# Kernel optimization log

Measured on AMD Instinct MI355X. Metric: run time of the kernel, lower is better.

The kernel has to match this reference:

```python
import jax, jax.numpy as jnp
import numpy as np

N, E, B = 50000, 800000, 128
IN, HID, OUT, H = 256, 256, 256, 4
NEG_SLOPE = 0.2
EPS_BN = 1e-5
EPS_LN = 1e-5


def setup_inputs() -> dict:
    key = jax.random.key(0)
    ks = jax.random.split(key, 10)
    C1, C2 = HID // H, OUT // H
    s = lambda k, sh: jax.random.normal(k, sh, jnp.float32) * 0.05
    return dict(
        x=jax.random.normal(ks[0], (N, IN), jnp.float32),
        edge_index=jax.random.randint(ks[1], (2, E), 0, N),
        batch=jnp.sort(jax.random.randint(ks[2], (N,), 0, B)),
        W1=s(ks[3], (IN, HID)), a_src1=s(ks[4], (H, C1)), a_dst1=s(ks[5], (H, C1)),
        b1=jnp.zeros((HID,), jnp.float32),
        bn1_g=jnp.ones((HID,), jnp.float32), bn1_b=jnp.zeros((HID,), jnp.float32),
        bn1_m=jnp.zeros((HID,), jnp.float32), bn1_v=jnp.ones((HID,), jnp.float32),
        ln1_g=jnp.ones((HID,), jnp.float32), ln1_b=jnp.zeros((HID,), jnp.float32),
        W2=s(ks[6], (HID + IN, OUT)), a_src2=s(ks[7], (H, C2)), a_dst2=s(ks[8], (H, C2)),
        b2=jnp.zeros((OUT,), jnp.float32),
        bn2_g=jnp.ones((OUT,), jnp.float32), bn2_b=jnp.zeros((OUT,), jnp.float32),
        bn2_m=jnp.zeros((OUT,), jnp.float32), bn2_v=jnp.ones((OUT,), jnp.float32),
        ln2_g=jnp.ones((OUT,), jnp.float32), ln2_b=jnp.zeros((OUT,), jnp.float32),
    )


def gat_conv(x, edge_index, W, a_s, a_d, b):
    # PyG GATConv (concat heads, add_self_loops=True, eval -> no attention dropout)
    n = x.shape[0]
    Hh, C = a_s.shape
    h = (x @ W).reshape(n, Hh, C)                      # [N,H,C]
    loop = jnp.arange(n)
    src = jnp.concatenate([edge_index[0], loop])       # [E+N]
    dst = jnp.concatenate([edge_index[1], loop])
    al_s = jnp.einsum('nhc,hc->nh', h, a_s)            # [N,H]
    al_d = jnp.einsum('nhc,hc->nh', h, a_d)
    e = jax.nn.leaky_relu(al_s[src] + al_d[dst], NEG_SLOPE)   # [E+N,H]
    emax = jax.ops.segment_max(e, dst, num_segments=n)        # segment softmax over incoming edges
    p = jnp.exp(e - emax[dst])
    denom = jax.ops.segment_sum(p, dst, num_segments=n)
    alpha = p / (denom[dst] + 1e-16)
    out = jax.ops.segment_sum(alpha[:, :, None] * h[src], dst, num_segments=n)
    return out.reshape(n, Hh * C) + b


def bn_eval(x, g, b, m, v):
    return (x - m) * (g * jax.lax.rsqrt(v + EPS_BN)) + b


def layer_norm(x, g, b):
    mu = jnp.mean(x, axis=-1, keepdims=True)
    var = jnp.mean(jnp.square(x - mu), axis=-1, keepdims=True)
    return (x - mu) * jax.lax.rsqrt(var + EPS_LN) * g + b


def reference(x, edge_index, batch,
              W1, a_src1, a_dst1, b1, bn1_g, bn1_b, bn1_m, bn1_v, ln1_g, ln1_b,
              W2, a_src2, a_dst2, b2, bn2_g, bn2_b, bn2_m, bn2_v, ln2_g, ln2_b):
    x1 = x
    h = gat_conv(x, edge_index, W1, a_src1, a_dst1, b1)
    h = jax.nn.relu(layer_norm(bn_eval(h, bn1_g, bn1_b, bn1_m, bn1_v), ln1_g, ln1_b))
    x2 = h
    # root_extend: broadcast the first node of each (sorted) batch segment
    root_idx = jnp.searchsorted(batch, jnp.arange(B))  # first occurrence per graph
    h = jnp.concatenate([h, x1[root_idx[batch]]], axis=1)
    h = gat_conv(h, edge_index, W2, a_src2, a_dst2, b2)
    h = jax.nn.relu(layer_norm(bn_eval(h, bn2_g, bn2_b, bn2_m, bn2_v), ln2_g, ln2_b))
    h = jnp.concatenate([h, x2[root_idx[batch]]], axis=1)   # [N, OUT+HID]
    sums = jax.ops.segment_sum(h, batch, num_segments=B)
    cnt = jax.ops.segment_sum(jnp.ones((h.shape[0],), h.dtype), batch, num_segments=B)
    return sums / jnp.maximum(cnt, 1.0)[:, None]            # scatter_mean -> [B, OUT+HID]
```

## Files before the change

kernel.cpp:

```cpp
#include <hip/hip_runtime.h>
#include <stdint.h>

typedef unsigned short u16;
typedef unsigned int u32;
typedef __bf16 bf16x8 __attribute__((ext_vector_type(8)));
typedef float f32x4 __attribute__((ext_vector_type(4)));

#define NGRAPH 128

__device__ __forceinline__ float b2f(u16 u) {
    union { u32 i; float f; } c; c.i = ((u32)u) << 16; return c.f;
}
__device__ __forceinline__ u16 f2b(float f) {
    union { float f; u32 i; } c; c.f = f;
    u32 r = c.i + 0x7fffu + ((c.i >> 16) & 1u);
    return (u16)(r >> 16);
}

__global__ void k_sentinel(u16* __restrict__ out, int n, u16 pat) {
    int i = blockIdx.x * 256 + threadIdx.x;
    if (i < n) out[i] = pat;
}

__global__ void k_detect(const u16* __restrict__ x, int* __restrict__ flag) {
    __shared__ int cnt;
    if (threadIdx.x == 0) cnt = 0;
    __syncthreads();
    int weird = 0;
    for (int i = threadIdx.x; i < 4096; i += 256) {
        u16 u = x[2 * i];
        int e = (u >> 7) & 0xff;
        if (e != 0 && (e < 100 || e > 140)) weird++;
    }
    atomicAdd(&cnt, weird);
    __syncthreads();
    if (threadIdx.x == 0) *flag = (cnt > 1024) ? 1 : 0;
}

__global__ __launch_bounds__(256) void k_cvt(const void* __restrict__ src, u16* __restrict__ dst,
                                             int n, const int* __restrict__ flag) {
    int f = *flag;
    int i = blockIdx.x * 256 + threadIdx.x;
    if (i < n) dst[i] = f ? f2b(((const float*)src)[i]) : ((const u16*)src)[i];
}

__global__ __launch_bounds__(256) void k_cvt_small(
    const void* p0, const void* p1, const void* p2, const void* p3, const void* p4,
    const void* p5, const void* p6, const void* p7, const void* p8, const void* p9,
    const void* p10, const void* p11, const void* p12, const void* p13, const void* p14,
    const void* p15, const void* p16, const void* p17,
    u16* __restrict__ dst, const int* __restrict__ flag) {
    const void* ps[18] = {p0,p1,p2,p3,p4,p5,p6,p7,p8,p9,p10,p11,p12,p13,p14,p15,p16,p17};
    int f = *flag;
    int vec = blockIdx.x;
    int j = threadIdx.x;
    const void* s = ps[vec];
    dst[vec * 256 + j] = f ? f2b(((const float*)s)[j]) : ((const u16*)s)[j];
}

__global__ void k_zero(int* __restrict__ deg, float* __restrict__ pool, int nd, int np) {
    int i = blockIdx.x * blockDim.x + threadIdx.x;
    if (i < nd) deg[i] = 0;
    if (i < np) pool[i] = 0.0f;
}

__global__ void k_transpose(const u16* __restrict__ w, u16* __restrict__ wt) {
    int idx = blockIdx.x * 256 + threadIdx.x;
    int n = idx >> 8, k = idx & 255;
    wt[n * 256 + k] = w[k * 256 + n];
}

__global__ void k_root(const int* __restrict__ batch, int* __restrict__ root, int N, int B) {
    int b = threadIdx.x;
    if (b > B) return;
    int lo = 0, hi = N;
    while (lo < hi) { int mid = (lo + hi) >> 1; if (batch[mid] < b) lo = mid + 1; else hi = mid; }
    root[b] = lo;
}

__global__ __launch_bounds__(256) void k_hist(const int* __restrict__ ei, int* __restrict__ deg, int E) {
    int e = blockIdx.x * 256 + threadIdx.x;
    if (e < E) atomicAdd(&deg[ei[E + e]], 1);
}

__global__ __launch_bounds__(256) void k_scan1(const int* __restrict__ in, int* __restrict__ out,
                                               int* __restrict__ bsums, int total) {
    __shared__ int lds[256];
    int tid = threadIdx.x;
    int base = blockIdx.x * 2048 + tid * 8;
    int v[8]; int ts = 0;
#pragma unroll
    for (int r = 0; r < 8; r++) { int i = base + r; int x = (i < total) ? in[i] : 0; v[r] = x; ts += x; }
    lds[tid] = ts;
    __syncthreads();
    for (int off = 1; off < 256; off <<= 1) {
        int t = (tid >= off) ? lds[tid - off] : 0;
        __syncthreads();
        lds[tid] += t;
        __syncthreads();
    }
    int run = lds[tid] - ts;
#pragma unroll
    for (int r = 0; r < 8; r++) { int i = base + r; if (i < total) out[i] = run; run += v[r]; }
    if (tid == 255) bsums[blockIdx.x] = lds[255];
}

__global__ void k_scan2(int* __restrict__ bsums, int nb) {
    if (threadIdx.x == 0 && blockIdx.x == 0) {
        int run = 0;
        for (int i = 0; i < nb; i++) { int t = bsums[i]; bsums[i] = run; run += t; }
    }
}

__global__ __launch_bounds__(256) void k_scan3(const int* __restrict__ pscan, const int* __restrict__ bsums,
                                               int* __restrict__ ptr, int* __restrict__ cursor,
                                               int total, int N) {
    int i = blockIdx.x * 256 + threadIdx.x;
    if (i >= total) return;
    int val = pscan[i] + bsums[i >> 11];
    ptr[i] = val;
    if (i < N) cursor[i] = val;
}

__global__ __launch_bounds__(256) void k_fill(const int* __restrict__ ei, int* __restrict__ cursor,
                                              int* __restrict__ csr, int E) {
    int e = blockIdx.x * 256 + threadIdx.x;
    if (e < E) {
        int src = ei[e];
        int pos = atomicAdd(&cursor[ei[E + e]], 1);
        csr[pos] = src;
    }
}

__global__ __launch_bounds__(256) void k_gemm(const u16* __restrict__ A, const u16* __restrict__ Bt,
                                              u16* __restrict__ C, int M,
                                              const float* __restrict__ r2, const int* __restrict__ batch) {
    __shared__ __align__(16) u16 As[128 * 64];
    __shared__ __align__(16) u16 Bs[128 * 64];
    const int tid = threadIdx.x;
    const int lane = tid & 63;
    const int wave = tid >> 6;
    const int bm = blockIdx.x >> 1;
    const int bn = blockIdx.x & 1;
    const int m0 = bm * 128, n0 = bn * 128;
    const int wm = wave >> 1, wn = wave & 1;
    const int lm = lane & 15, lq = lane >> 4;
    f32x4 acc[4][4] = {};

    for (int k0 = 0; k0 < 256; k0 += 64) {
        uint4 ra[4], rb[4];
#pragma unroll
        for (int it = 0; it < 4; ++it) {
            int t = tid + 256 * it;
            int m = t >> 3;
            int kc = (t & 7) ^ (m & 7);
            int gm = m0 + m; if (gm > M - 1) gm = M - 1;
            ra[it] = *(const uint4*)(A + (size_t)gm * 256 + k0 + kc * 8);
            rb[it] = *(const uint4*)(Bt + (size_t)(n0 + m) * 256 + k0 + kc * 8);
        }
        __syncthreads();
#pragma unroll
        for (int it = 0; it < 4; ++it) {
            int t = tid + 256 * it;
            *(uint4*)(As + t * 8) = ra[it];
            *(uint4*)(Bs + t * 8) = rb[it];
        }
        __syncthreads();
#pragma unroll
        for (int ks = 0; ks < 2; ++ks) {
            int kq = ks * 4 + lq;
            bf16x8 af[4], bfr[4];
#pragma unroll
            for (int i = 0; i < 4; i++) {
                int m = wm * 64 + i * 16 + lm;
                af[i] = *(const bf16x8*)(As + (m * 8 + (kq ^ (m & 7))) * 8);
                int n = wn * 64 + i * 16 + lm;
                bfr[i] = *(const bf16x8*)(Bs + (n * 8 + (kq ^ (n & 7))) * 8);
            }
#pragma unroll
            for (int i = 0; i < 4; i++)
#pragma unroll
                for (int j = 0; j < 4; j++)
                    acc[i][j] = __builtin_amdgcn_mfma_f32_16x16x32_bf16(af[i], bfr[j], acc[i][j], 0, 0, 0);
        }
    }
#pragma unroll
    for (int i = 0; i < 4; i++) {
#pragma unroll
        for (int r = 0; r < 4; r++) {
            int row = m0 + wm * 64 + i * 16 + lq * 4 + r;
            if (row >= M) continue;
            const float* r2row = r2 ? (r2 + (size_t)batch[row] * 256) : nullptr;
#pragma unroll
            for (int j = 0; j < 4; j++) {
                int col = n0 + wn * 64 + j * 16 + lm;
                float v = acc[i][j][r];
                if (r2row) v += r2row[col];
                C[(size_t)row * 256 + col] = f2b(v);
            }
        }
    }
}

__global__ __launch_bounds__(256) void k_al(const u16* __restrict__ h, const u16* __restrict__ a_s,
                                            const u16* __restrict__ a_d,
                                            float* __restrict__ al_s, float* __restrict__ al_d, int N) {
    int node = blockIdx.x * 4 + (threadIdx.x >> 6);
    if (node >= N) return;
    int lane = threadIdx.x & 63;
    int c0 = lane * 4;
    int head = lane >> 4;
    int ci = c0 & 63;
    ushort4 hv = *(const ushort4*)(h + (size_t)node * 256 + c0);
    float h0 = b2f(hv.x), h1 = b2f(hv.y), h2 = b2f(hv.z), h3 = b2f(hv.w);
    ushort4 sv = *(const ushort4*)(a_s + head * 64 + ci);
    ushort4 dv = *(const ushort4*)(a_d + head * 64 + ci);
    float ps = h0 * b2f(sv.x) + h1 * b2f(sv.y) + h2 * b2f(sv.z) + h3 * b2f(sv.w);
    float pd = h0 * b2f(dv.x) + h1 * b2f(dv.y) + h2 * b2f(dv.z) + h3 * b2f(dv.w);
#pragma unroll
    for (int off = 1; off < 16; off <<= 1) { ps += __shfl_xor(ps, off); pd += __shfl_xor(pd, off); }
    if ((lane & 15) == 0) { al_s[node * 4 + head] = ps; al_d[node * 4 + head] = pd; }
}

__global__ __launch_bounds__(256) void k_attw(
    const float* __restrict__ als, const float* __restrict__ ald_,
    const int* __restrict__ ptr, const int* __restrict__ csr,
    float* __restrict__ aw, float* __restrict__ selfp, float* __restrict__ invs, int N) {
    int node = blockIdx.x * 4 + (threadIdx.x >> 6);
    if (node >= N) return;
    int lane = threadIdx.x & 63;
    int hd = lane & 3;
    int el = lane >> 2;
    int beg = ptr[node], end = ptr[node + 1];
    float ad = ald_[node * 4 + hd];
    float es = als[node * 4 + hd] + ad; es = (es > 0.f) ? es : 0.2f * es;
    float m = es;
    for (int i0 = beg; i0 < end; i0 += 16) {
        int i = i0 + el;
        if (i < end) {
            int src = csr[i];
            float e2 = als[src * 4 + hd] + ad; e2 = (e2 > 0.f) ? e2 : 0.2f * e2;
            m = fmaxf(m, e2);
        }
    }
#pragma unroll
    for (int off = 4; off < 64; off <<= 1) m = fmaxf(m, __shfl_xor(m, off));
    float s = 0.f;
    for (int i0 = beg; i0 < end; i0 += 16) {
        int i = i0 + el;
        if (i < end) {
            int src = csr[i];
            float e2 = als[src * 4 + hd] + ad; e2 = (e2 > 0.f) ? e2 : 0.2f * e2;
            float p = __expf(e2 - m);
            aw[(size_t)i * 4 + hd] = p;
            s += p;
        }
    }
#pragma unroll
    for (int off = 4; off < 64; off <<= 1) s += __shfl_xor(s, off);
    float pself = __expf(es - m);
    s += pself;
    if (el == 0) {
        float inv = 1.0f / (s + 1e-16f);
        selfp[node * 4 + hd] = pself * inv;
        invs[node * 4 + hd] = inv;
    }
}

__global__ __launch_bounds__(256) void k_agg2(
    const u16* __restrict__ h, const float* __restrict__ aw,
    const float* __restrict__ selfp, const float* __restrict__ invs,
    const int* __restrict__ ptr, const int* __restrict__ csr,
    const u16* __restrict__ bias, const u16* __restrict__ bng, const u16* __restrict__ bnb,
    const u16* __restrict__ bnm, const u16* __restrict__ bnv,
    const u16* __restrict__ lng, const u16* __restrict__ lnb,
    u16* __restrict__ xout, float* __restrict__ pool, const int* __restrict__ batch, int N) {
    int node = blockIdx.x * 4 + (threadIdx.x >> 6);
    if (node >= N) return;
    int lane = threadIdx.x & 63;
    int c0 = lane * 4;
    int head = lane >> 4;
    int beg = ptr[node], end = ptr[node + 1];
    float a0 = 0.f, a1 = 0.f, a2 = 0.f, a3 = 0.f;
    int i = beg;
    for (; i + 4 <= end; i += 4) {
        int s0 = csr[i], s1 = csr[i + 1], s2 = csr[i + 2], s3 = csr[i + 3];
        float p0 = aw[(size_t)i * 4 + head];
        float p1 = aw[(size_t)(i + 1) * 4 + head];
        float p2 = aw[(size_t)(i + 2) * 4 + head];
        float p3 = aw[(size_t)(i + 3) * 4 + head];
        ushort4 r0 = *(const ushort4*)(h + (size_t)s0 * 256 + c0);
        ushort4 r1 = *(const ushort4*)(h + (size_t)s1 * 256 + c0);
        ushort4 r2v = *(const ushort4*)(h + (size_t)s2 * 256 + c0);
        ushort4 r3 = *(const ushort4*)(h + (size_t)s3 * 256 + c0);
        a0 += p0 * b2f(r0.x) + p1 * b2f(r1.x) + p2 * b2f(r2v.x) + p3 * b2f(r3.x);
        a1 += p0 * b2f(r0.y) + p1 * b2f(r1.y) + p2 * b2f(r2v.y) + p3 * b2f(r3.y);
        a2 += p0 * b2f(r0.z) + p1 * b2f(r1.z) + p2 * b2f(r2v.z) + p3 * b2f(r3.z);
        a3 += p0 * b2f(r0.w) + p1 * b2f(r1.w) + p2 * b2f(r2v.w) + p3 * b2f(r3.w);
    }
    for (; i < end; ++i) {
        int s0 = csr[i];
        float p0 = aw[(size_t)i * 4 + head];
        ushort4 r0 = *(const ushort4*)(h + (size_t)s0 * 256 + c0);
        a0 += p0 * b2f(r0.x); a1 += p0 * b2f(r0.y); a2 += p0 * b2f(r0.z); a3 += p0 * b2f(r0.w);
    }
    float inv = invs[node * 4 + head];
    float sp = selfp[node * 4 + head];
    ushort4 hs = *(const ushort4*)(h + (size_t)node * 256 + c0);
    float v0 = a0 * inv + sp * b2f(hs.x) + b2f(bias[c0 + 0]);
    float v1 = a1 * inv + sp * b2f(hs.y) + b2f(bias[c0 + 1]);
    float v2 = a2 * inv + sp * b2f(hs.z) + b2f(bias[c0 + 2]);
    float v3 = a3 * inv + sp * b2f(hs.w) + b2f(bias[c0 + 3]);
    v0 = (v0 - b2f(bnm[c0 + 0])) * (b2f(bng[c0 + 0]) * rsqrtf(b2f(bnv[c0 + 0]) + 1e-5f)) + b2f(bnb[c0 + 0]);
    v1 = (v1 - b2f(bnm[c0 + 1])) * (b2f(bng[c0 + 1]) * rsqrtf(b2f(bnv[c0 + 1]) + 1e-5f)) + b2f(bnb[c0 + 1]);
    v2 = (v2 - b2f(bnm[c0 + 2])) * (b2f(bng[c0 + 2]) * rsqrtf(b2f(bnv[c0 + 2]) + 1e-5f)) + b2f(bnb[c0 + 2]);
    v3 = (v3 - b2f(bnm[c0 + 3])) * (b2f(bng[c0 + 3]) * rsqrtf(b2f(bnv[c0 + 3]) + 1e-5f)) + b2f(bnb[c0 + 3]);
    float sum = v0 + v1 + v2 + v3;
#pragma unroll
    for (int off = 1; off < 64; off <<= 1) sum += __shfl_xor(sum, off);
    float mu = sum * 0.00390625f;
    float d0 = v0 - mu, d1 = v1 - mu, d2 = v2 - mu, d3 = v3 - mu;
    float q = d0 * d0 + d1 * d1 + d2 * d2 + d3 * d3;
#pragma unroll
    for (int off = 1; off < 64; off <<= 1) q += __shfl_xor(q, off);
    float rstd = rsqrtf(q * 0.00390625f + 1e-5f);
    float y0 = fmaxf(d0 * rstd * b2f(lng[c0 + 0]) + b2f(lnb[c0 + 0]), 0.f);
    float y1 = fmaxf(d1 * rstd * b2f(lng[c0 + 1]) + b2f(lnb[c0 + 1]), 0.f);
    float y2 = fmaxf(d2 * rstd * b2f(lng[c0 + 2]) + b2f(lnb[c0 + 2]), 0.f);
    float y3 = fmaxf(d3 * rstd * b2f(lng[c0 + 3]) + b2f(lnb[c0 + 3]), 0.f);
    if (xout) {
        uint2 o;
        o.x = (u32)f2b(y0) | ((u32)f2b(y1) << 16);
        o.y = (u32)f2b(y2) | ((u32)f2b(y3) << 16);
        *(uint2*)(xout + (size_t)node * 256 + c0) = o;
    }
    if (pool) {
        int g = batch[node];
        float* pp = pool + (size_t)g * 256 + c0;
        atomicAdd(pp + 0, y0); atomicAdd(pp + 1, y1); atomicAdd(pp + 2, y2); atomicAdd(pp + 3, y3);
    }
}

__global__ __launch_bounds__(256) void k_r2(const u16* __restrict__ xc, const u16* __restrict__ w2,
                                            const int* __restrict__ root, float* __restrict__ r2, int N) {
    __shared__ float xs[256];
    int b = blockIdx.x, c = threadIdx.x;
    int rt = root[b]; if (rt >= N) rt = N - 1; if (rt < 0) rt = 0;
    xs[c] = b2f(xc[(size_t)rt * 256 + c]);
    __syncthreads();
    float acc = 0.f;
    for (int k = 0; k < 256; k++) acc += xs[k] * b2f(w2[(size_t)(256 + k) * 256 + c]);
    r2[b * 256 + c] = acc;
}

__global__ void k_final(const float* __restrict__ pool, const u16* __restrict__ x2,
                        const int* __restrict__ root, void* __restrict__ out,
                        const int* __restrict__ flag) {
    int b = blockIdx.x, c = threadIdx.x;
    int r0 = root[b], r1 = root[b + 1];
    int cnt = r1 - r0;
    float inv = 1.0f / (float)(cnt > 1 ? cnt : 1);
    float v0 = pool[b * 256 + c] * inv;
    float v1 = (cnt > 0) ? b2f(x2[(size_t)r0 * 256 + c]) : 0.0f;
    if (*flag) {
        float* o = (float*)out;
        o[b * 512 + c] = v0;
        o[b * 512 + 256 + c] = v1;
    } else {
        u16* o = (u16*)out;
        o[b * 512 + c] = f2b(v0);
        o[b * 512 + 256 + c] = f2b(v1);
    }
}

extern "C" void kernel_launch(void* const* d_in, const int* in_sizes, int n_in,
                              void* d_out, int out_size, void* d_ws, size_t ws_size,
                              hipStream_t stream) {
    u16* outp = (u16*)d_out;
    int ogrid = (out_size + 255) / 256;

    if (n_in != 23) {
        k_sentinel<<<ogrid, 256, 0, stream>>>(outp, out_size, (u16)0x44FA);
        return;
    }

    const void* x_raw = d_in[0];
    const int* ei = (const int*)d_in[1];
    const int* batch = (const int*)d_in[2];
    const int NX = in_sizes[0];
    const int E = in_sizes[1] / 2;
    const int N = in_sizes[2];
    const int NW1 = in_sizes[3];
    const int NW2 = in_sizes[13];
    const int B = NGRAPH;

    char* p = (char*)d_ws;
    auto carve = [&](size_t bytes) -> void* {
        void* r = (void*)p; p += (bytes + 255) & ~(size_t)255; return r;
    };
    u16* xc    = (u16*)carve((size_t)NX * 2);
    u16* w1c   = (u16*)carve((size_t)NW1 * 2);
    u16* w2c   = (u16*)carve((size_t)NW2 * 2);
    u16* sc    = (u16*)carve((size_t)18 * 256 * 2);
    u16* wt1   = (u16*)carve((size_t)65536 * 2);
    u16* wt2   = (u16*)carve((size_t)65536 * 2);
    u16* hbuf  = (u16*)carve((size_t)N * 256 * 2);
    u16* x2    = (u16*)carve((size_t)N * 256 * 2);
    float* als = (float*)carve((size_t)N * 4 * 4);
    float* ald = (float*)carve((size_t)N * 4 * 4);
    float* aw  = (float*)carve((size_t)E * 4 * 4);
    float* sfp = (float*)carve((size_t)N * 4 * 4);
    float* ivs = (float*)carve((size_t)N * 4 * 4);
    int* deg    = (int*)carve((size_t)(N + 1) * 4);
    int* pscan  = (int*)carve((size_t)(N + 1) * 4);
    int* ptr    = (int*)carve((size_t)(N + 1) * 4);
    int* cursor = (int*)carve((size_t)N * 4);
    int* csr    = (int*)carve((size_t)E * 4);
    int* bsums  = (int*)carve(1024);
    int* root   = (int*)carve((size_t)(B + 1) * 4);
    float* r2   = (float*)carve((size_t)B * 256 * 4);
    float* pool = (float*)carve((size_t)B * 256 * 4);
    int* flag   = (int*)carve(256);

    size_t needed = (size_t)(p - (char*)d_ws);
    if (needed > ws_size) {
        k_sentinel<<<ogrid, 256, 0, stream>>>(outp, out_size, (u16)0x447A);
        return;
    }

    k_detect<<<1, 256, 0, stream>>>((const u16*)x_raw, flag);

    int zmax = (N + 1) > (B * 256) ? (N + 1) : (B * 256);
    k_zero<<<(zmax + 255) / 256, 256, 0, stream>>>(deg, pool, N + 1, B * 256);

    k_cvt<<<(NX + 255) / 256, 256, 0, stream>>>(x_raw, xc, NX, flag);
    k_cvt<<<(NW1 + 255) / 256, 256, 0, stream>>>(d_in[3], w1c, NW1, flag);
    k_cvt<<<(NW2 + 255) / 256, 256, 0, stream>>>(d_in[13], w2c, NW2, flag);
    k_cvt_small<<<18, 256, 0, stream>>>(
        d_in[4], d_in[5], d_in[6], d_in[7], d_in[8], d_in[9], d_in[10], d_in[11], d_in[12],
        d_in[14], d_in[15], d_in[16], d_in[17], d_in[18], d_in[19], d_in[20], d_in[21], d_in[22],
        sc, flag);

    k_transpose<<<256, 256, 0, stream>>>(w1c, wt1);
    k_transpose<<<256, 256, 0, stream>>>(w2c, wt2);
    k_root<<<1, 256, 0, stream>>>(batch, root, N, B);

    k_hist<<<(E + 255) / 256, 256, 0, stream>>>(ei, deg, E);
    int nb1 = (N + 1 + 2047) / 2048;
    k_scan1<<<nb1, 256, 0, stream>>>(deg, pscan, bsums, N + 1);
    k_scan2<<<1, 64, 0, stream>>>(bsums, nb1);
    k_scan3<<<(N + 1 + 255) / 256, 256, 0, stream>>>(pscan, bsums, ptr, cursor, N + 1, N);
    k_fill<<<(E + 255) / 256, 256, 0, stream>>>(ei, cursor, csr, E);

    int mt = (N + 127) / 128;
    int ngrid = (N + 3) / 4;
    k_gemm<<<mt * 2, 256, 0, stream>>>(xc, wt1, hbuf, N, nullptr, nullptr);
    k_al<<<ngrid, 256, 0, stream>>>(hbuf, sc + 0 * 256, sc + 1 * 256, als, ald, N);
    k_attw<<<ngrid, 256, 0, stream>>>(als, ald, ptr, csr, aw, sfp, ivs, N);
    k_agg2<<<ngrid, 256, 0, stream>>>(hbuf, aw, sfp, ivs, ptr, csr,
        sc + 2 * 256, sc + 3 * 256, sc + 4 * 256, sc + 5 * 256, sc + 6 * 256, sc + 7 * 256, sc + 8 * 256,
        x2, nullptr, batch, N);
    k_r2<<<B, 256, 0, stream>>>(xc, w2c, root, r2, N);
    k_gemm<<<mt * 2, 256, 0, stream>>>(x2, wt2, hbuf, N, r2, batch);
    k_al<<<ngrid, 256, 0, stream>>>(hbuf, sc + 9 * 256, sc + 10 * 256, als, ald, N);
    k_attw<<<ngrid, 256, 0, stream>>>(als, ald, ptr, csr, aw, sfp, ivs, N);
    k_agg2<<<ngrid, 256, 0, stream>>>(hbuf, aw, sfp, ivs, ptr, csr,
        sc + 11 * 256, sc + 12 * 256, sc + 13 * 256, sc + 14 * 256, sc + 15 * 256, sc + 16 * 256, sc + 17 * 256,
        nullptr, pool, batch, N);

    k_final<<<B, 256, 0, stream>>>(pool, x2, root, d_out, flag);
    (void)ws_size;
}
```

Measured before the change: 795.4 us.

## Quantize GEMM output to int8 per head, fuse softmax into aggregation, merge setup kernels

The GEMM epilogue now also writes an int8 copy of h with one scale per row per 64-column head group, stored next to the source attention logit. Edge weights are computed inside the aggregation kernel with an unnormalised exp, and the separate attention-weight pass and its per-edge buffer are removed. Neighbour gathers then read int8 rows instead of bf16, about half the bytes. The small setup kernels (detect, zero, root, convert, transpose) are merged into fewer launches. The risks are int8 quantisation error and dropping the max-subtraction, which can overflow exp for large logits.

After: 1.061 ms. 33.4% more time.

```diff
diff --git a/kernel.cpp b/kernel.cpp
--- a/kernel.cpp
+++ b/kernel.cpp
@@ -3,6 +3,7 @@
 
 typedef unsigned short u16;
 typedef unsigned int u32;
+typedef unsigned char u8;
 typedef __bf16 bf16x8 __attribute__((ext_vector_type(8)));
 typedef float f32x4 __attribute__((ext_vector_type(4)));
 
@@ -16,66 +17,81 @@
     u32 r = c.i + 0x7fffu + ((c.i >> 16) & 1u);
     return (u16)(r >> 16);
 }
+__device__ __forceinline__ float s8x(u32 v, int k) {
+    return (float)((int)(v << (24 - 8 * k)) >> 24);
+}
 
 __global__ void k_sentinel(u16* __restrict__ out, int n, u16 pat) {
     int i = blockIdx.x * 256 + threadIdx.x;
     if (i < n) out[i] = pat;
 }
 
-__global__ void k_detect(const u16* __restrict__ x, int* __restrict__ flag) {
+__global__ __launch_bounds__(256) void k_init(const u16* __restrict__ x, const int* __restrict__ batch,
+                                              int* __restrict__ deg, float* __restrict__ pool,
+                                              int* __restrict__ flag, int* __restrict__ root,
+                                              int N, int B) {
     __shared__ int cnt;
-    if (threadIdx.x == 0) cnt = 0;
-    __syncthreads();
-    int weird = 0;
-    for (int i = threadIdx.x; i < 4096; i += 256) {
-        u16 u = x[2 * i];
-        int e = (u >> 7) & 0xff;
-        if (e != 0 && (e < 100 || e > 140)) weird++;
-    }
-    atomicAdd(&cnt, weird);
-    __syncthreads();
-    if (threadIdx.x == 0) *flag = (cnt > 1024) ? 1 : 0;
-}
-
-__global__ __launch_bounds__(256) void k_cvt(const void* __restrict__ src, u16* __restrict__ dst,
-                                             int n, const int* __restrict__ flag) {
-    int f = *flag;
     int i = blockIdx.x * 256 + threadIdx.x;
-    if (i < n) dst[i] = f ? f2b(((const float*)src)[i]) : ((const u16*)src)[i];
-}
-
-__global__ __launch_bounds__(256) void k_cvt_small(
+    if (i < N + 1) deg[i] = 0;
+    if (i < B * 256) pool[i] = 0.0f;
+    if (blockIdx.x == 0) {
+        if (threadIdx.x == 0) cnt = 0;
+        __syncthreads();
+        int weird = 0;
+        for (int k = threadIdx.x; k < 4096; k += 256) {
+            u16 u = x[2 * k];
+            int e = (u >> 7) & 0xff;
+            if (e != 0 && (e < 100 || e > 140)) weird++;
+        }
+        atomicAdd(&cnt, weird);
+        __syncthreads();
+        if (threadIdx.x == 0) *flag = (cnt > 1024) ? 1 : 0;
+    } else if (blockIdx.x == 1) {
+        int b = threadIdx.x;
+        if (b <= B) {
+            int lo = 0, hi = N;
+            while (lo < hi) { int mid = (lo + hi) >> 1; if (batch[mid] < b) lo = mid + 1; else hi = mid; }
+            root[b] = lo;
+        }
+    }
+}
+
+__global__ __launch_bounds__(256) void k_convert(
+    const void* __restrict__ x, const void* __restrict__ w1, const void* __restrict__ w2,
     const void* p0, const void* p1, const void* p2, const void* p3, const void* p4,
     const void* p5, const void* p6, const void* p7, const void* p8, const void* p9,
     const void* p10, const void* p11, const void* p12, const void* p13, const void* p14,
     const void* p15, const void* p16, const void* p17,
-    u16* __restrict__ dst, const int* __restrict__ flag) {
+    u16* __restrict__ xc, u16* __restrict__ w1c, u16* __restrict__ w2c, u16* __restrict__ sc,
+    int nx, int nw1, int nw2, const int* __restrict__ flag) {
     const void* ps[18] = {p0,p1,p2,p3,p4,p5,p6,p7,p8,p9,p10,p11,p12,p13,p14,p15,p16,p17};
     int f = *flag;
-    int vec = blockIdx.x;
-    int j = threadIdx.x;
-    const void* s = ps[vec];
-    dst[vec * 256 + j] = f ? f2b(((const float*)s)[j]) : ((const u16*)s)[j];
-}
-
-__global__ void k_zero(int* __restrict__ deg, float* __restrict__ pool, int nd, int np) {
-    int i = blockIdx.x * blockDim.x + threadIdx.x;
-    if (i < nd) deg[i] = 0;
-    if (i < np) pool[i] = 0.0f;
-}
-
-__global__ void k_transpose(const u16* __restrict__ w, u16* __restrict__ wt) {
+    long long i = (long long)blockIdx.x * 256 + threadIdx.x;
+    long long t0 = nx, t1 = t0 + nw1, t2 = t1 + nw2, t3 = t2 + 18 * 256;
+    if (i < t0) {
+        xc[i] = f ? f2b(((const float*)x)[i]) : ((const u16*)x)[i];
+    } else if (i < t1) {
+        long long j = i - t0;
+        w1c[j] = f ? f2b(((const float*)w1)[j]) : ((const u16*)w1)[j];
+    } else if (i < t2) {
+        long long j = i - t1;
+        w2c[j] = f ? f2b(((const float*)w2)[j]) : ((const u16*)w2)[j];
+    } else if (i < t3) {
+        long long k = i - t2;
+        const void* s = ps[k >> 8];
+        int j = (int)(k & 255);
+        sc[k] = f ? f2b(((const float*)s)[j]) : ((const u16*)s)[j];
+    }
+}
+
+__global__ __launch_bounds__(256) void k_tr2(const u16* __restrict__ w1, u16* __restrict__ wt1,
+                                             const u16* __restrict__ w2, u16* __restrict__ wt2) {
     int idx = blockIdx.x * 256 + threadIdx.x;
-    int n = idx >> 8, k = idx & 255;
-    wt[n * 256 + k] = w[k * 256 + n];
-}
-
-__global__ void k_root(const int* __restrict__ batch, int* __restrict__ root, int N, int B) {
-    int b = threadIdx.x;
-    if (b > B) return;
-    int lo = 0, hi = N;
-    while (lo < hi) { int mid = (lo + hi) >> 1; if (batch[mid] < b) lo = mid + 1; else hi = mid; }
-    root[b] = lo;
+    int halfsel = idx >> 16;
+    int j = idx & 65535;
+    int n = j >> 8, k = j & 255;
+    if (halfsel == 0) wt1[n * 256 + k] = w1[k * 256 + n];
+    else              wt2[n * 256 + k] = w2[k * 256 + n];
 }
 
 __global__ __launch_bounds__(256) void k_hist(const int* __restrict__ ei, int* __restrict__ deg, int E) {
@@ -133,10 +149,12 @@
 }
 
 __global__ __launch_bounds__(256) void k_gemm(const u16* __restrict__ A, const u16* __restrict__ Bt,
-                                              u16* __restrict__ C, int M,
+                                              u16* __restrict__ C, u8* __restrict__ C8,
+                                              float* __restrict__ salsc, int M,
                                               const float* __restrict__ r2, const int* __restrict__ batch) {
-    __shared__ __align__(16) u16 As[128 * 64];
-    __shared__ __align__(16) u16 Bs[128 * 64];
+    __shared__ __align__(16) u16 smem[128 * 64 * 2];
+    u16* As = smem;
+    u16* Bs = smem + 128 * 64;
     const int tid = threadIdx.x;
     const int lane = tid & 63;
     const int wave = tid >> 6;
@@ -184,27 +202,51 @@
                     acc[i][j] = __builtin_amdgcn_mfma_f32_16x16x32_bf16(af[i], bfr[j], acc[i][j], 0, 0, 0);
         }
     }
+
+    __syncthreads();
+    u8* lds8 = (u8*)smem;
 #pragma unroll
     for (int i = 0; i < 4; i++) {
 #pragma unroll
         for (int r = 0; r < 4; r++) {
-            int row = m0 + wm * 64 + i * 16 + lq * 4 + r;
-            if (row >= M) continue;
-            const float* r2row = r2 ? (r2 + (size_t)batch[row] * 256) : nullptr;
+            int rl = wm * 64 + i * 16 + lq * 4 + r;
+            int row = m0 + rl;
+            bool ok = (row < M);
+            const float* r2row = (r2 && ok) ? (r2 + (size_t)batch[row] * 256) : nullptr;
+            float v[4];
+#pragma unroll
+            for (int j = 0; j < 4; j++) {
+                v[j] = acc[i][j][r];
+                if (r2row) v[j] += r2row[n0 + wn * 64 + j * 16 + lm];
+            }
+            float mx = fmaxf(fmaxf(fabsf(v[0]), fabsf(v[1])), fmaxf(fabsf(v[2]), fabsf(v[3])));
+#pragma unroll
+            for (int off = 1; off < 16; off <<= 1) mx = fmaxf(mx, __shfl_xor(mx, off));
+            float scl = mx * (1.0f / 127.0f);
+            float isc = (mx > 0.f) ? 127.0f / mx : 0.f;
 #pragma unroll
             for (int j = 0; j < 4; j++) {
                 int col = n0 + wn * 64 + j * 16 + lm;
-                float v = acc[i][j][r];
-                if (r2row) v += r2row[col];
-                C[(size_t)row * 256 + col] = f2b(v);
+                if (ok) C[(size_t)row * 256 + col] = f2b(v[j]);
+                int q = (int)rintf(v[j] * isc);
+                lds8[rl * 144 + wn * 64 + j * 16 + lm] = (u8)(q & 0xff);
             }
-        }
+            if (ok && lm == 0) salsc[(size_t)row * 8 + (bn * 2 + wn) * 2 + 1] = scl;
+        }
+    }
+    __syncthreads();
+    for (int t = tid; t < 1024; t += 256) {
+        int rl = t >> 3;
+        int off = (t & 7) * 16;
+        int row = m0 + rl;
+        if (row < M)
+            *(uint4*)(C8 + (size_t)row * 256 + n0 + off) = *(const uint4*)(lds8 + rl * 144 + off);
     }
 }
 
 __global__ __launch_bounds__(256) void k_al(const u16* __restrict__ h, const u16* __restrict__ a_s,
                                             const u16* __restrict__ a_d,
-                                            float* __restrict__ al_s, float* __restrict__ al_d, int N) {
+                                            float* __restrict__ salsc, float* __restrict__ ald, int N) {
     int node = blockIdx.x * 4 + (threadIdx.x >> 6);
     if (node >= N) return;
     int lane = threadIdx.x & 63;
@@ -219,57 +261,15 @@
     float pd = h0 * b2f(dv.x) + h1 * b2f(dv.y) + h2 * b2f(dv.z) + h3 * b2f(dv.w);
 #pragma unroll
     for (int off = 1; off < 16; off <<= 1) { ps += __shfl_xor(ps, off); pd += __shfl_xor(pd, off); }
-    if ((lane & 15) == 0) { al_s[node * 4 + head] = ps; al_d[node * 4 + head] = pd; }
-}
-
-__global__ __launch_bounds__(256) void k_attw(
-    const float* __restrict__ als, const float* __restrict__ ald_,
-    const int* __restrict__ ptr, const int* __restrict__ csr,
-    float* __restrict__ aw, float* __restrict__ selfp, float* __restrict__ invs, int N) {
-    int node = blockIdx.x * 4 + (threadIdx.x >> 6);
-    if (node >= N) return;
-    int lane = threadIdx.x & 63;
-    int hd = lane & 3;
-    int el = lane >> 2;
-    int beg = ptr[node], end = ptr[node + 1];
-    float ad = ald_[node * 4 + hd];
-    float es = als[node * 4 + hd] + ad; es = (es > 0.f) ? es : 0.2f * es;
-    float m = es;
-    for (int i0 = beg; i0 < end; i0 += 16) {
-        int i = i0 + el;
-        if (i < end) {
-            int src = csr[i];
-            float e2 = als[src * 4 + hd] + ad; e2 = (e2 > 0.f) ? e2 : 0.2f * e2;
-            m = fmaxf(m, e2);
-        }
-    }
-#pragma unroll
-    for (int off = 4; off < 64; off <<= 1) m = fmaxf(m, __shfl_xor(m, off));
-    float s = 0.f;
-    for (int i0 = beg; i0 < end; i0 += 16) {
-        int i = i0 + el;
-        if (i < end) {
-            int src = csr[i];
-            float e2 = als[src * 4 + hd] + ad; e2 = (e2 > 0.f) ? e2 : 0.2f * e2;
-            float p = __expf(e2 - m);
-            aw[(size_t)i * 4 + hd] = p;
-            s += p;
-        }
-    }
-#pragma unroll
-    for (int off = 4; off < 64; off <<= 1) s += __shfl_xor(s, off);
-    float pself = __expf(es - m);
-    s += pself;
-    if (el == 0) {
-        float inv = 1.0f / (s + 1e-16f);
-        selfp[node * 4 + hd] = pself * inv;
-        invs[node * 4 + hd] = inv;
-    }
-}
-
-__global__ __launch_bounds__(256) void k_agg2(
-    const u16* __restrict__ h, const float* __restrict__ aw,
-    const float* __restrict__ selfp, const float* __restrict__ invs,
+    if ((lane & 15) == 0) {
+        salsc[(size_t)node * 8 + head * 2] = ps;
+        ald[node * 4 + head] = pd;
+    }
+}
+
+__global__ __launch_bounds__(256) void k_agg5(
+    const u16* __restrict__ h, const u8* __restrict__ h8,
+    const float* __restrict__ salsc, const float* __restrict__ ald_,
     const int* __restrict__ ptr, const int* __restrict__ csr,
     const u16* __restrict__ bias, const u16* __restrict__ bng, const u16* __restrict__ bnb,
     const u16* __restrict__ bnm, const u16* __restrict__ bnv,
@@ -280,37 +280,51 @@
     int lane = threadIdx.x & 63;
     int c0 = lane * 4;
     int head = lane >> 4;
+    float ad = ald_[node * 4 + head];
+    float es = salsc[(size_t)node * 8 + head * 2] + ad; es = (es > 0.f) ? es : 0.2f * es;
+    float psf = __expf(es);
+    float s = psf;
+    ushort4 hv = *(const ushort4*)(h + (size_t)node * 256 + c0);
+    float a0 = psf * b2f(hv.x), a1 = psf * b2f(hv.y), a2 = psf * b2f(hv.z), a3 = psf * b2f(hv.w);
     int beg = ptr[node], end = ptr[node + 1];
-    float a0 = 0.f, a1 = 0.f, a2 = 0.f, a3 = 0.f;
     int i = beg;
     for (; i + 4 <= end; i += 4) {
         int s0 = csr[i], s1 = csr[i + 1], s2 = csr[i + 2], s3 = csr[i + 3];
-        float p0 = aw[(size_t)i * 4 + head];
-        float p1 = aw[(size_t)(i + 1) * 4 + head];
-        float p2 = aw[(size_t)(i + 2) * 4 + head];
-        float p3 = aw[(size_t)(i + 3) * 4 + head];
-        ushort4 r0 = *(const ushort4*)(h + (size_t)s0 * 256 + c0);
-        ushort4 r1 = *(const ushort4*)(h + (size_t)s1 * 256 + c0);
-        ushort4 r2v = *(const ushort4*)(h + (size_t)s2 * 256 + c0);
-        ushort4 r3 = *(const ushort4*)(h + (size_t)s3 * 256 + c0);
-        a0 += p0 * b2f(r0.x) + p1 * b2f(r1.x) + p2 * b2f(r2v.x) + p3 * b2f(r3.x);
-        a1 += p0 * b2f(r0.y) + p1 * b2f(r1.y) + p2 * b2f(r2v.y) + p3 * b2f(r3.y);
-        a2 += p0 * b2f(r0.z) + p1 * b2f(r1.z) + p2 * b2f(r2v.z) + p3 * b2f(r3.z);
-        a3 += p0 * b2f(r0.w) + p1 * b2f(r1.w) + p2 * b2f(r2v.w) + p3 * b2f(r3.w);
+        float2 f0 = *(const float2*)(salsc + (size_t)s0 * 8 + head * 2);
+        float2 f1 = *(const float2*)(salsc + (size_t)s1 * 8 + head * 2);
+        float2 f2v = *(const float2*)(salsc + (size_t)s2 * 8 + head * 2);
+        float2 f3 = *(const float2*)(salsc + (size_t)s3 * 8 + head * 2);
+        u32 r0 = *(const u32*)(h8 + (size_t)s0 * 256 + c0);
+        u32 r1 = *(const u32*)(h8 + (size_t)s1 * 256 + c0);
+        u32 r2v = *(const u32*)(h8 + (size_t)s2 * 256 + c0);
+        u32 r3 = *(const u32*)(h8 + (size_t)s3 * 256 + c0);
+        float e0 = f0.x + ad; e0 = (e0 > 0.f) ? e0 : 0.2f * e0;
+        float e1 = f1.x + ad; e1 = (e1 > 0.f) ? e1 : 0.2f * e1;
+        float e2 = f2v.x + ad; e2 = (e2 > 0.f) ? e2 : 0.2f * e2;
+        float e3 = f3.x + ad; e3 = (e3 > 0.f) ? e3 : 0.2f * e3;
+        float p0 = __expf(e0), p1 = __expf(e1), p2 = __expf(e2), p3 = __expf(e3);
+        s += p0 + p1 + p2 + p3;
+        float w0 = p0 * f0.y, w1 = p1 * f1.y, w2 = p2 * f2v.y, w3 = p3 * f3.y;
+        a0 += w0 * s8x(r0, 0) + w1 * s8x(r1, 0) + w2 * s8x(r2v, 0) + w3 * s8x(r3, 0);
+        a1 += w0 * s8x(r0, 1) + w1 * s8x(r1, 1) + w2 * s8x(r2v, 1) + w3 * s8x(r3, 1);
+        a2 += w0 * s8x(r0, 2) + w1 * s8x(r1, 2) + w2 * s8x(r2v, 2) + w3 * s8x(r3, 2);
+        a3 += w0 * s8x(r0, 3) + w1 * s8x(r1, 3) + w2 * s8x(r2v, 3) + w3 * s8x(r3, 3);
     }
     for (; i < end; ++i) {
         int s0 = csr[i];
-        float p0 = aw[(size_t)i * 4 + head];
-        ushort4 r0 = *(const ushort4*)(h + (size_t)s0 * 256 + c0);
-        a0 += p0 * b2f(r0.x); a1 += p0 * b2f(r0.y); a2 += p0 * b2f(r0.z); a3 += p0 * b2f(r0.w);
-    }
-    float inv = invs[node * 4 + head];
-    float sp = selfp[node * 4 + head];
-    ushort4 hs = *(const ushort4*)(h + (size_t)node * 256 + c0);
-    float v0 = a0 * inv + sp * b2f(hs.x) + b2f(bias[c0 + 0]);
-    float v1 = a1 * inv + sp * b2f(hs.y) + b2f(bias[c0 + 1]);
-    float v2 = a2 * inv + sp * b2f(hs.z) + b2f(bias[c0 + 2]);
-    float v3 = a3 * inv + sp * b2f(hs.w) + b2f(bias[c0 + 3]);
+        float2 f0 = *(const float2*)(salsc + (size_t)s0 * 8 + head * 2);
+        u32 r0 = *(const u32*)(h8 + (size_t)s0 * 256 + c0);
+        float e0 = f0.x + ad; e0 = (e0 > 0.f) ? e0 : 0.2f * e0;
+        float p0 = __expf(e0);
+        s += p0;
+        float w0 = p0 * f0.y;
+        a0 += w0 * s8x(r0, 0); a1 += w0 * s8x(r0, 1); a2 += w0 * s8x(r0, 2); a3 += w0 * s8x(r0, 3);
+    }
+    float inv = 1.0f / (s + 1e-16f);
+    float v0 = a0 * inv + b2f(bias[c0 + 0]);
+    float v1 = a1 * inv + b2f(bias[c0 + 1]);
+    float v2 = a2 * inv + b2f(bias[c0 + 2]);
+    float v3 = a3 * inv + b2f(bias[c0 + 3]);
     v0 = (v0 - b2f(bnm[c0 + 0])) * (b2f(bng[c0 + 0]) * rsqrtf(b2f(bnv[c0 + 0]) + 1e-5f)) + b2f(bnb[c0 + 0]);
     v1 = (v1 - b2f(bnm[c0 + 1])) * (b2f(bng[c0 + 1]) * rsqrtf(b2f(bnv[c0 + 1]) + 1e-5f)) + b2f(bnb[c0 + 1]);
     v2 = (v2 - b2f(bnm[c0 + 2])) * (b2f(bng[c0 + 2]) * rsqrtf(b2f(bnv[c0 + 2]) + 1e-5f)) + b2f(bnb[c0 + 2]);
@@ -405,12 +419,10 @@
     u16* wt1   = (u16*)carve((size_t)65536 * 2);
     u16* wt2   = (u16*)carve((size_t)65536 * 2);
     u16* hbuf  = (u16*)carve((size_t)N * 256 * 2);
+    u8*  h8    = (u8*)carve((size_t)N * 256);
     u16* x2    = (u16*)carve((size_t)N * 256 * 2);
-    float* als = (float*)carve((size_t)N * 4 * 4);
+    float* salsc = (float*)carve((size_t)N * 8 * 4);
     float* ald = (float*)carve((size_t)N * 4 * 4);
-    float* aw  = (float*)carve((size_t)E * 4 * 4);
-    float* sfp = (float*)carve((size_t)N * 4 * 4);
-    float* ivs = (float*)carve((size_t)N * 4 * 4);
     int* deg    = (int*)carve((size_t)(N + 1) * 4);
     int* pscan  = (int*)carve((size_t)(N + 1) * 4);
     int* ptr    = (int*)carve((size_t)(N + 1) * 4);
@@ -428,22 +440,17 @@
         return;
     }
 
-    k_detect<<<1, 256, 0, stream>>>((const u16*)x_raw, flag);
-
     int zmax = (N + 1) > (B * 256) ? (N + 1) : (B * 256);
-    k_zero<<<(zmax + 255) / 256, 256, 0, stream>>>(deg, pool, N + 1, B * 256);
-
-    k_cvt<<<(NX + 255) / 256, 256, 0, stream>>>(x_raw, xc, NX, flag);
-    k_cvt<<<(NW1 + 255) / 256, 256, 0, stream>>>(d_in[3], w1c, NW1, flag);
-    k_cvt<<<(NW2 + 255) / 256, 256, 0, stream>>>(d_in[13], w2c, NW2, flag);
-    k_cvt_small<<<18, 256, 0, stream>>>(
+    k_init<<<(zmax + 255) / 256, 256, 0, stream>>>((const u16*)x_raw, batch, deg, pool, flag, root, N, B);
+
+    long long tot = (long long)NX + NW1 + NW2 + 18 * 256;
+    k_convert<<<(unsigned)((tot + 255) / 256), 256, 0, stream>>>(
+        x_raw, d_in[3], d_in[13],
         d_in[4], d_in[5], d_in[6], d_in[7], d_in[8], d_in[9], d_in[10], d_in[11], d_in[12],
         d_in[14], d_in[15], d_in[16], d_in[17], d_in[18], d_in[19], d_in[20], d_in[21], d_in[22],
-        sc, flag);
-
-    k_transpose<<<256, 256, 0, stream>>>(w1c, wt1);
-    k_transpose<<<256, 256, 0, stream>>>(w2c, wt2);
-    k_root<<<1, 256, 0, stream>>>(batch, root, N, B);
+        xc, w1c, w2c, sc, NX, NW1, NW2, flag);
+
+    k_tr2<<<512, 256, 0, stream>>>(w1c, wt1, w2c, wt2);
 
     k_hist<<<(E + 255) / 256, 256, 0, stream>>>(ei, deg, E);
     int nb1 = (N + 1 + 2047) / 2048;
@@ -454,17 +461,15 @@
 
     int mt = (N + 127) / 128;
     int ngrid = (N + 3) / 4;
-    k_gemm<<<mt * 2, 256, 0, stream>>>(xc, wt1, hbuf, N, nullptr, nullptr);
-    k_al<<<ngrid, 256, 0, stream>>>(hbuf, sc + 0 * 256, sc + 1 * 256, als, ald, N);
-    k_attw<<<ngrid, 256, 0, stream>>>(als, ald, ptr, csr, aw, sfp, ivs, N);
-    k_agg2<<<ngrid, 256, 0, stream>>>(hbuf, aw, sfp, ivs, ptr, csr,
+    k_gemm<<<mt * 2, 256, 0, stream>>>(xc, wt1, hbuf, h8, salsc, N, nullptr, nullptr);
+    k_al<<<ngrid, 256, 0, stream>>>(hbuf, sc + 0 * 256, sc + 1 * 256, salsc, ald, N);
+    k_agg5<<<ngrid, 256, 0, stream>>>(hbuf, h8, salsc, ald, ptr, csr,
         sc + 2 * 256, sc + 3 * 256, sc + 4 * 256, sc + 5 * 256, sc + 6 * 256, sc + 7 * 256, sc + 8 * 256,
         x2, nullptr, batch, N);
     k_r2<<<B, 256, 0, stream>>>(xc, w2c, root, r2, N);
-    k_gemm<<<mt * 2, 256, 0, stream>>>(x2, wt2, hbuf, N, r2, batch);
-    k_al<<<ngrid, 256, 0, stream>>>(hbuf, sc + 9 * 256, sc + 10 * 256, als, ald, N);
-    k_attw<<<ngrid, 256, 0, stream>>>(als, ald, ptr, csr, aw, sfp, ivs, N);
-    k_agg2<<<ngrid, 256, 0, stream>>>(hbuf, aw, sfp, ivs, ptr, csr,
+    k_gemm<<<mt * 2, 256, 0, stream>>>(x2, wt2, hbuf, h8, salsc, N, r2, batch);
+    k_al<<<ngrid, 256, 0, stream>>>(hbuf, sc + 9 * 256, sc + 10 * 256, salsc, ald, N);
+    k_agg5<<<ngrid, 256, 0, stream>>>(hbuf, h8, salsc, ald, ptr, csr,
         sc + 11 * 256, sc + 12 * 256, sc + 13 * 256, sc + 14 * 256, sc + 15 * 256, sc + 16 * 256, sc + 17 * 256,
         nullptr, pool, batch, N);
 
```
